# Kernel tuning notes

Measured on AMD Instinct MI355X. Metric: run time of the kernel, lower is better.

Reference implementation:

```python
import jax, jax.numpy as jnp
import numpy as np

# Production GravNet config: 8 events x 4096 hits, K=40 neighbours, 4 spatial dims
B, V, K, S, P, F_IN, F_OUT = 8, 4096, 40, 4, 64, 64, 128
N = B * V
MAX_RADIUS_SQ = 1.0  # SelectKnn(max_radius=1.0)


def setup_inputs() -> dict:
    key = jax.random.key(0)
    ks = jax.random.split(key, 7)
    x = jax.random.normal(ks[0], (N, F_IN), jnp.float32)
    # Dense layer params (glorot-ish scaling)
    W_prop = jax.random.normal(ks[1], (F_IN, P), jnp.float32) / np.sqrt(F_IN)
    b_prop = jnp.zeros((P,), jnp.float32)
    W_sp = jax.random.normal(ks[2], (F_IN, S), jnp.float32) / np.sqrt(F_IN)
    b_sp = jnp.zeros((S,), jnp.float32)
    # output transform input dim = n_prop_total (2*P) + F_IN
    W_out = jax.random.normal(ks[3], (2 * P + F_IN, F_OUT), jnp.float32) / np.sqrt(2 * P + F_IN)
    b_out = jnp.zeros((F_OUT,), jnp.float32)
    row_splits = jnp.arange(B + 1, dtype=jnp.int32) * V  # equal-size ragged segments
    return dict(x=x, W_prop=W_prop, b_prop=b_prop, W_sp=W_sp, b_sp=b_sp,
                W_out=W_out, b_out=b_out, row_splits=row_splits)


def _knn_indices(coords):
    """Per-event brute-force KNN. coords: [N,S] -> global neighbour idx [N,K]."""
    c = coords.reshape(B, V, S)
    # pairwise squared distances within each event: [B,V,V]
    d = jnp.sum((c[:, :, None, :] - c[:, None, :, :]) ** 2, axis=-1)
    neg_d, idx = jax.lax.top_k(-d, K + 1)  # nearest first; col 0 is self (d=0)
    idx, dsq = idx[:, :, 1:], -neg_d[:, :, 1:]
    # tf_compatible max_radius: out-of-radius neighbours -> self index
    self_idx = jnp.arange(V, dtype=idx.dtype)[None, :, None]
    idx = jnp.where(dsq > MAX_RADIUS_SQ, self_idx, idx)
    gidx = idx + (jnp.arange(B, dtype=idx.dtype) * V)[:, None, None]
    return gidx.reshape(N, K)


def reference(x, W_prop, b_prop, W_sp, b_sp, W_out, b_out, row_splits):
    coords = x @ W_sp + b_sp                      # [N,S] learned coordinates
    nidx = _knn_indices(coords)                   # [N,K] (int, non-diff)
    nb_coords = coords[nidx]                      # [N,K,S] gather
    dsq = jnp.sum((coords[:, None, :] - nb_coords) ** 2, axis=-1)  # [N,K]
    feat = x @ W_prop + b_prop                    # [N,P]
    w = jnp.exp(-10.0 * dsq)[:, :, None]          # gauss_of_lin(10*d^2)
    nf = feat[nidx] * w                           # [N,K,P]
    agg = jnp.concatenate([nf.max(axis=1), nf.mean(axis=1)], axis=-1)  # [N,2P]
    out = jnp.tanh(jnp.concatenate([agg, x], axis=-1) @ W_out + b_out)  # [N,F_OUT]
    return out
```

## Files before the change

### kernel.cpp

```cpp
#include <hip/hip_runtime.h>
#include <cstdint>
#include <cstddef>

#define NB   8
#define VV   4096
#define KNN  40
#define NTOT 32768
#define CAP  224
#define INFB 0x7F800000u
#define ONEB 0x3F800000u

__device__ __forceinline__ int slabf(float x) {
  int b = (int)floorf((x + 4.f) * 2.f);
  return b < 0 ? 0 : (b > 15 ? 15 : b);
}
__device__ __forceinline__ int ybf(float y) {
  int b = (int)floorf((y + 4.f) * 4.f);
  return b < 0 ? 0 : (b > 31 ? 31 : b);
}

__global__ __launch_bounds__(256) void k_prep(
    const float* __restrict__ x, const float* __restrict__ W_prop,
    const float* __restrict__ b_prop, const float* __restrict__ W_sp,
    const float* __restrict__ b_sp, const float* __restrict__ W_out,
    float* __restrict__ coords, float* __restrict__ feat,
    float* __restrict__ xW, int* __restrict__ hist)
{
  __shared__ float xt[64][64];
  const int t = threadIdx.x;
  const int row0 = blockIdx.x * 64;

  #pragma unroll
  for (int i = 0; i < 16; ++i) {
    int idx = t + i * 256;
    xt[idx >> 6][idx & 63] = x[(size_t)row0 * 64 + idx];
  }
  __syncthreads();

  {
    const int col = t & 63, rb = (t >> 6) * 16;
    float acc[16];
    #pragma unroll
    for (int i = 0; i < 16; ++i) acc[i] = b_prop[col];
    for (int k = 0; k < 64; k += 4) {
      const float w0 = W_prop[(k + 0) * 64 + col];
      const float w1 = W_prop[(k + 1) * 64 + col];
      const float w2 = W_prop[(k + 2) * 64 + col];
      const float w3 = W_prop[(k + 3) * 64 + col];
      #pragma unroll
      for (int i = 0; i < 16; ++i) {
        const float4 a4 = *(const float4*)&xt[rb + i][k];
        acc[i] += a4.x * w0 + a4.y * w1 + a4.z * w2 + a4.w * w3;
      }
    }
    #pragma unroll
    for (int i = 0; i < 16; ++i)
      feat[(size_t)(row0 + rb + i) * 64 + col] = acc[i];
  }

  {
    const int col = t & 127, who = t >> 7;
    #pragma unroll
    for (int p = 0; p < 2; ++p) {
      const int rb = who * 16 + p * 32;
      float acc[16];
      #pragma unroll
      for (int i = 0; i < 16; ++i) acc[i] = 0.f;
      for (int k = 0; k < 64; k += 4) {
        const float w0 = W_out[(size_t)(128 + k + 0) * 128 + col];
        const float w1 = W_out[(size_t)(128 + k + 1) * 128 + col];
        const float w2 = W_out[(size_t)(128 + k + 2) * 128 + col];
        const float w3 = W_out[(size_t)(128 + k + 3) * 128 + col];
        #pragma unroll
        for (int i = 0; i < 16; ++i) {
          const float4 a4 = *(const float4*)&xt[rb + i][k];
          acc[i] += a4.x * w0 + a4.y * w1 + a4.z * w2 + a4.w * w3;
        }
      }
      #pragma unroll
      for (int i = 0; i < 16; ++i)
        xW[(size_t)(row0 + rb + i) * 128 + col] = acc[i];
    }
  }

  if (t < 64) {
    float a0 = b_sp[0], a1 = b_sp[1], a2 = b_sp[2], a3 = b_sp[3];
    for (int k = 0; k < 64; ++k) {
      const float xv = xt[t][k];
      a0 += xv * W_sp[k * 4 + 0];
      a1 += xv * W_sp[k * 4 + 1];
      a2 += xv * W_sp[k * 4 + 2];
      a3 += xv * W_sp[k * 4 + 3];
    }
    ((float4*)coords)[row0 + t] = make_float4(a0, a1, a2, a3);
    const int ev = (row0 + t) >> 12;
    atomicAdd(&hist[ev * 512 + slabf(a0) * 32 + ybf(a1)], 1);
  }
}

__global__ __launch_bounds__(512) void k_scatter(
    const float* __restrict__ coords, float* __restrict__ csort,
    unsigned short* __restrict__ perm, const int* __restrict__ hist,
    int* __restrict__ cursorDelta, unsigned short* __restrict__ prefg)
{
  __shared__ int pref[513];
  const int t = threadIdx.x;
  const int ev = blockIdx.x >> 3;
  const int i = ((blockIdx.x & 7) << 9) + t;
  const int evbase = ev * VV;

  if (t < 64) {
    const int l = t;
    const int* h = hist + ev * 512 + 8 * l;
    int hv[8], s = 0;
    #pragma unroll
    for (int j = 0; j < 8; ++j) { hv[j] = h[j]; s += hv[j]; }
    int incl = s;
    #pragma unroll
    for (int off = 1; off < 64; off <<= 1) {
      const int v = __shfl_up(incl, off);
      if (l >= off) incl += v;
    }
    int run = incl - s;
    #pragma unroll
    for (int j = 0; j < 8; ++j) { pref[8 * l + j] = run; run += hv[j]; }
    if (l == 63) pref[512] = run;
  }
  __syncthreads();

  const float4 c = ((const float4*)coords)[evbase + i];
  const int key = slabf(c.x) * 32 + ybf(c.y);
  const int pos = pref[key] + atomicAdd(&cursorDelta[ev * 512 + key], 1);
  ((float4*)csort)[evbase + pos] = c;
  perm[evbase + pos] = (unsigned short)i;

  if ((blockIdx.x & 7) == 0) {
    prefg[ev * 513 + t] = (unsigned short)pref[t];
    if (t == 0) prefg[ev * 513 + 512] = (unsigned short)pref[512];
  }
}

template <int NC>
__device__ __forceinline__ unsigned bs40(const uint2* __restrict__ list,
                                         int M, int lane) {
  unsigned dv[NC];
  #pragma unroll
  for (int j = 0; j < NC; ++j) {
    const int e = lane + j * 64;
    dv[j] = (e < M) ? list[e].x : INFB;
  }
  unsigned lo = 0, hi = ONEB;
  while (lo < hi) {
    const unsigned mid = (lo + hi) >> 1;
    int cnt = 0;
    #pragma unroll
    for (int j = 0; j < NC; ++j)
      cnt += (int)__popcll(__ballot(dv[j] <= mid));
    if (cnt >= KNN) hi = mid; else lo = mid + 1;
  }
  return hi;
}

#define AGG_CHUNK(J0, N)                                                     \
  {                                                                          \
    float fv[N], wgt[N];                                                     \
    _Pragma("unroll")                                                        \
    for (int j = 0; j < N; ++j) {                                            \
      const uint2 en = list[(J0) + j];              \
      wgt[j] = __expf(-10.f * __uint_as_float(en.x));                        \
      const int ei = __builtin_amdgcn_readfirstlane((int)en.y);              \
      fv[j] = fe[(size_t)ei * 64 + lane];        \
    }                                                                        \
    _Pragma("unroll")                                                        \
    for (int j = 0; j < N; ++j) {                                            \
      const float v = fv[j] * wgt[j];                                        \
      vmax = fmaxf(vmax, v);                                                 \
      vsum += v;                                                             \
    }                                                                        \
  }

__global__ __launch_bounds__(512, 4) void k_knn(
    const float* __restrict__ coords,
    const unsigned short* __restrict__ perm,
    const unsigned short* __restrict__ prefg,
    const float* __restrict__ feat, float* __restrict__ agg,
    const float* __restrict__ W_out, const float* __restrict__ b_out,
    float* __restrict__ out)
{
  __shared__ float4 cs[VV];
  __shared__ uint2 lists[8][CAP];
  __shared__ unsigned short pr[513];
  __shared__ unsigned short origq_s[64];

  const int t = threadIdx.x, lane = t & 63;
  const int wvid = __builtin_amdgcn_readfirstlane(t) >> 6;
  const int bid0 = blockIdx.x;
  const int bid = (bid0 & 7) * 64 + (bid0 >> 3);
  const int ev = bid >> 6;
  const int slot = bid & 63;
  const int evbase = ev * VV;

  {
    const float4* cg = (const float4*)coords + evbase;
    for (int i = t; i < VV; i += 512) cs[i] = cg[i];
    for (int i = t; i < 513; i += 512) pr[i] = prefg[ev * 513 + i];
  }
  __syncthreads();

  uint2* list = lists[wvid];
  const float* fe = feat + (size_t)evbase * 64;
  const unsigned long long lmask = (1ull << lane) - 1ull;

  auto scanAll = [&](unsigned rbits, int q, float4 qc,
                     int slo, int shi, int yblo, int ybhi) -> int {
    int M = 0, pend = 0;
    for (int s = slo; s <= shi; ++s) {
      int alo = ((int)pr[(s << 5) + yblo]) & ~63;
      int ahi = (((int)pr[(s << 5) + ybhi + 1]) + 63) & ~63;
      alo = alo < pend ? pend : alo;
      if (ahi < alo) ahi = alo;
      pend = ahi;
      #pragma unroll 4
      for (int base = alo; base < ahi; base += 64) {
        const int c = base + lane;
        const float4 cc = cs[c];
        const float dx = qc.x - cc.x, dy = qc.y - cc.y;
        const float dz = qc.z - cc.z, dw = qc.w - cc.w;
        const float dsq = dx * dx + dy * dy + dz * dz + dw * dw;
        const bool pred = (__float_as_uint(dsq) <= rbits) && (c != q);
        const unsigned long long bm = __ballot(pred);
        if (pred) {
          const int pos = M + (int)__popcll(bm & lmask);
          if (pos < CAP)
            list[pos] = make_uint2(__float_as_uint(dsq), (unsigned)c);
        }
        M += (int)__popcll(bm);
      }
    }
    return M;
  };

  for (int qi = 0; qi < 8; ++qi) {
    const int q = slot + (qi * 8 + wvid) * 64;
    const float4 qc = cs[q];
    const int origq = (int)perm[evbase + q];
    if (lane == 0) origq_s[qi * 8 + wvid] = (unsigned short)origq;
    const int slo = slabf(qc.x - 1.f), shi = slabf(qc.x + 1.f);
    const int yblo = ybf(qc.y - 1.f),  ybhi = ybf(qc.y + 1.f);

    int M = scanAll(ONEB, q, qc, slo, shi, yblo, ybhi);
    bool ok = true;

    if (M > CAP) {
      const unsigned t0 = bs40<4>(list, CAP, lane);
      M = scanAll(t0, q, qc, slo, shi, yblo, ybhi);
      ok = (M <= CAP);
    }

    float vmax = -__builtin_inff(), vsum = 0.f;

    if (ok) {
      for (int be = 0; be < M; be += 64) {
        const int e = be + lane;
        if (e < M) {
          uint2 en = list[e];
          en.y = (unsigned)perm[evbase + (int)en.y];
          list[e] = en;
        }
      }

      int Msel;
      if (M > KNN) {
        unsigned taub;
        if      (M <=  64) taub = bs40<1>(list, M, lane);
        else if (M <= 128) taub = bs40<2>(list, M, lane);
        else               taub = bs40<4>(list, M, lane);
        int S = 0;
        for (int be = 0; be < M; be += 64) {
          const int e = be + lane;
          uint2 en = make_uint2(0u, 0u);
          bool p = false;
          if (e < M) { en = list[e]; p = (en.x <= taub); }
          const unsigned long long bm = __ballot(p);
          if (p) list[S + (int)__popcll(bm & lmask)] = en;
          S += (int)__popcll(bm);
        }
        Msel = S;
      } else {
        if (lane >= M && lane < KNN)
          list[lane] = make_uint2(0u, (unsigned)origq);
        Msel = KNN;
      }

      if (Msel == KNN) {
        AGG_CHUNK(0, 16)
        AGG_CHUNK(16, 16)
        AGG_CHUNK(32, 8)
      } else {
        #pragma unroll 4
        for (int e = 0; e < Msel; ++e) {
          const uint2 en = list[e];
          const int ei = __builtin_amdgcn_readfirstlane((int)en.y);
          const float w = __expf(-10.f * __uint_as_float(en.x));
          const float v = fe[(size_t)ei * 64 + lane] * w;
          vmax = fmaxf(vmax, v);
          vsum += v;
        }
      }
    } else {
      unsigned lo = 0, hi = ONEB;
      while (lo < hi) {
        const unsigned mid = (lo + hi) >> 1;
        const float fm = __uint_as_float(mid);
        int cnt = 0, pend = 0;
        for (int s = slo; s <= shi; ++s) {
          int alo = ((int)pr[(s << 5) + yblo]) & ~63;
          int ahi = (((int)pr[(s << 5) + ybhi + 1]) + 63) & ~63;
          alo = alo < pend ? pend : alo;
          if (ahi < alo) ahi = alo;
          pend = ahi;
          for (int base = alo; base < ahi; base += 64) {
            const int c = base + lane;
            const float4 cc = cs[c];
            const float dx = qc.x - cc.x, dy = qc.y - cc.y;
            const float dz = qc.z - cc.z, dw = qc.w - cc.w;
            const float dsq = dx * dx + dy * dy + dz * dz + dw * dw;
            cnt += (int)__popcll(__ballot(dsq <= fm && c != q));
          }
        }
        if (cnt >= KNN) hi = mid; else lo = mid + 1;
      }
      const float tau = __uint_as_float(hi);
      int pend = 0;
      for (int s = slo; s <= shi; ++s) {
        int alo = ((int)pr[(s << 5) + yblo]) & ~63;
        int ahi = (((int)pr[(s << 5) + ybhi + 1]) + 63) & ~63;
        alo = alo < pend ? pend : alo;
        if (ahi < alo) ahi = alo;
        pend = ahi;
        for (int c = alo; c < ahi; ++c) {
          if (c == q) continue;
          const float4 cc = cs[c];
          const float dx = qc.x - cc.x, dy = qc.y - cc.y;
          const float dz = qc.z - cc.z, dw = qc.w - cc.w;
          const float dsq = dx * dx + dy * dy + dz * dz + dw * dw;
          if (dsq <= tau) {
            const int ei = (int)perm[evbase + c];
            const float w = __expf(-10.f * dsq);
            const float v = fe[(size_t)ei * 64 + lane] * w;
            vmax = fmaxf(vmax, v);
            vsum += v;
          }
        }
      }
    }

    const int g = evbase + origq;
    agg[(size_t)g * 128 + lane]      = vmax;
    agg[(size_t)g * 128 + 64 + lane] = vsum * (1.f / 40.f);
  }

  __syncthreads();
  float* aggS = (float*)cs;
  #pragma unroll
  for (int p = 0; p < 4; ++p) {
    const int idx = t + p * 512;
    const int row = idx >> 5, seg = idx & 31;
    const int g = evbase + (int)origq_s[row];
    ((float4*)aggS)[idx] = *(const float4*)&agg[(size_t)g * 128 + seg * 4];
  }
  __syncthreads();

  {
    const int col = t & 127, who = t >> 7;
    float acc[16];
    #pragma unroll
    for (int i = 0; i < 16; ++i) acc[i] = 0.f;
    for (int k = 0; k < 128; k += 4) {
      const float w0 = W_out[(size_t)(k + 0) * 128 + col];
      const float w1 = W_out[(size_t)(k + 1) * 128 + col];
      const float w2 = W_out[(size_t)(k + 2) * 128 + col];
      const float w3 = W_out[(size_t)(k + 3) * 128 + col];
      #pragma unroll
      for (int i = 0; i < 16; ++i) {
        const float4 a4 = *(const float4*)&aggS[(who * 16 + i) * 128 + k];
        acc[i] += a4.x * w0 + a4.y * w1 + a4.z * w2 + a4.w * w3;
      }
    }
    const float bb = b_out[col];
    #pragma unroll
    for (int i = 0; i < 16; ++i) {
      const int row = who * 16 + i;
      const size_t o = ((size_t)evbase + origq_s[row]) * 128 + col;
      float v = acc[i] + bb + out[o];
      v = fminf(15.f, fmaxf(-15.f, v));
      const float e = __expf(2.f * v);
      out[o] = (e - 1.f) / (e + 1.f);
    }
  }
}

extern "C" void kernel_launch(void* const* d_in, const int* in_sizes, int n_in,
                              void* d_out, int out_size, void* d_ws, size_t ws_size,
                              hipStream_t stream) {
  const float* x      = (const float*)d_in[0];
  const float* W_prop = (const float*)d_in[1];
  const float* b_prop = (const float*)d_in[2];
  const float* W_sp   = (const float*)d_in[3];
  const float* b_sp   = (const float*)d_in[4];
  const float* W_out  = (const float*)d_in[5];
  const float* b_out  = (const float*)d_in[6];

  float* out = (float*)d_out;
  char* ws = (char*)d_ws;
  float* coords          = (float*)(ws);
  float* csort           = (float*)(ws + (512 << 10));
  float* feat            = (float*)(ws + (1 << 20));
  float* agg             = (float*)(ws + (9 << 20));
  unsigned short* perm   = (unsigned short*)(ws + (25 << 20));
  unsigned short* prefg  = (unsigned short*)(ws + (25 << 20) + 65536);
  int* hist              = (int*)(ws + (25 << 20) + 65536 + 8704);
  int* cursorDelta       = (int*)(ws + (25 << 20) + 65536 + 8704 + 16384);

  hipMemsetAsync(hist, 0, 32768, stream);
  k_prep<<<NTOT / 64, 256, 0, stream>>>(x, W_prop, b_prop, W_sp, b_sp, W_out,
                                        coords, feat, out ,
                                        hist);
  k_scatter<<<NB * 8, 512, 0, stream>>>(coords, csort, perm, hist,
                                        cursorDelta, prefg);
  k_knn<<<NB * (VV / 64), 512, 0, stream>>>(csort, perm, prefg, feat, agg,
                                            W_out, b_out, out);
}
```

Measured before the change: 180.0 us.

## Read coords from global and keep aggregates in shared memory instead of workspace

Removes the per-block staging of all 4096 event coordinates into LDS. The KNN scans now read the sorted coordinates directly from global memory, relying on cache. The freed LDS holds the 64x128 aggregate tile written directly by each wave, which removes the global agg round-trip and one barrier. In exchange, the inner scan loops now issue global/cache loads in place of LDS reads, which could raise latency in the distance loops.

```diff
diff --git a/kernel.cpp b/kernel.cpp
--- a/kernel.cpp
+++ b/kernel.cpp
@@ -183,11 +183,11 @@
     const float* __restrict__ coords,
     const unsigned short* __restrict__ perm,
     const unsigned short* __restrict__ prefg,
-    const float* __restrict__ feat, float* __restrict__ agg,
+    const float* __restrict__ feat,
     const float* __restrict__ W_out, const float* __restrict__ b_out,
     float* __restrict__ out)
 {
-  __shared__ float4 cs[VV];
+  __shared__ float aggS[64 * 128];
   __shared__ uint2 lists[8][CAP];
   __shared__ unsigned short pr[513];
   __shared__ unsigned short origq_s[64];
@@ -200,11 +200,8 @@
   const int slot = bid & 63;
   const int evbase = ev * VV;
 
-  {
-    const float4* cg = (const float4*)coords + evbase;
-    for (int i = t; i < VV; i += 512) cs[i] = cg[i];
-    for (int i = t; i < 513; i += 512) pr[i] = prefg[ev * 513 + i];
-  }
+  const float4* cg = (const float4*)coords + evbase;
+  for (int i = t; i < 513; i += 512) pr[i] = prefg[ev * 513 + i];
   __syncthreads();
 
   uint2* list = lists[wvid];
@@ -223,7 +220,7 @@
       #pragma unroll 4
       for (int base = alo; base < ahi; base += 64) {
         const int c = base + lane;
-        const float4 cc = cs[c];
+        const float4 cc = cg[c];
         const float dx = qc.x - cc.x, dy = qc.y - cc.y;
         const float dz = qc.z - cc.z, dw = qc.w - cc.w;
         const float dsq = dx * dx + dy * dy + dz * dz + dw * dw;
@@ -242,7 +239,7 @@
 
   for (int qi = 0; qi < 8; ++qi) {
     const int q = slot + (qi * 8 + wvid) * 64;
-    const float4 qc = cs[q];
+    const float4 qc = cg[q];
     const int origq = (int)perm[evbase + q];
     if (lane == 0) origq_s[qi * 8 + wvid] = (unsigned short)origq;
     const int slo = slabf(qc.x - 1.f), shi = slabf(qc.x + 1.f);
@@ -321,7 +318,7 @@
           pend = ahi;
           for (int base = alo; base < ahi; base += 64) {
             const int c = base + lane;
-            const float4 cc = cs[c];
+            const float4 cc = cg[c];
             const float dx = qc.x - cc.x, dy = qc.y - cc.y;
             const float dz = qc.z - cc.z, dw = qc.w - cc.w;
             const float dsq = dx * dx + dy * dy + dz * dz + dw * dw;
@@ -340,7 +337,7 @@
         pend = ahi;
         for (int c = alo; c < ahi; ++c) {
           if (c == q) continue;
-          const float4 cc = cs[c];
+          const float4 cc = cg[c];
           const float dx = qc.x - cc.x, dy = qc.y - cc.y;
           const float dz = qc.z - cc.z, dw = qc.w - cc.w;
           const float dsq = dx * dx + dy * dy + dz * dz + dw * dw;
@@ -355,38 +352,29 @@
       }
     }
 
-    const int g = evbase + origq;
-    agg[(size_t)g * 128 + lane]      = vmax;
-    agg[(size_t)g * 128 + 64 + lane] = vsum * (1.f / 40.f);
+    const int row = qi * 8 + wvid;
+    aggS[row * 128 + lane]      = vmax;
+    aggS[row * 128 + 64 + lane] = vsum * (1.f / 40.f);
   }
 
   __syncthreads();
-  float* aggS = (float*)cs;
+
+  const int col = t & 127, who = t >> 7;
+  float acc[16];
   #pragma unroll
-  for (int p = 0; p < 4; ++p) {
-    const int idx = t + p * 512;
-    const int row = idx >> 5, seg = idx & 31;
-    const int g = evbase + (int)origq_s[row];
-    ((float4*)aggS)[idx] = *(const float4*)&agg[(size_t)g * 128 + seg * 4];
-  }
-  __syncthreads();
-
+  for (int i = 0; i < 16; ++i) acc[i] = 0.f;
+  for (int k = 0; k < 128; k += 4) {
+    const float w0 = W_out[(size_t)(k + 0) * 128 + col];
+    const float w1 = W_out[(size_t)(k + 1) * 128 + col];
+    const float w2 = W_out[(size_t)(k + 2) * 128 + col];
+    const float w3 = W_out[(size_t)(k + 3) * 128 + col];
+    #pragma unroll
+    for (int i = 0; i < 16; ++i) {
+      const float4 a4 = *(const float4*)&aggS[(who * 16 + i) * 128 + k];
+      acc[i] += a4.x * w0 + a4.y * w1 + a4.z * w2 + a4.w * w3;
+    }
+  }
   {
-    const int col = t & 127, who = t >> 7;
-    float acc[16];
-    #pragma unroll
-    for (int i = 0; i < 16; ++i) acc[i] = 0.f;
-    for (int k = 0; k < 128; k += 4) {
-      const float w0 = W_out[(size_t)(k + 0) * 128 + col];
-      const float w1 = W_out[(size_t)(k + 1) * 128 + col];
-      const float w2 = W_out[(size_t)(k + 2) * 128 + col];
-      const float w3 = W_out[(size_t)(k + 3) * 128 + col];
-      #pragma unroll
-      for (int i = 0; i < 16; ++i) {
-        const float4 a4 = *(const float4*)&aggS[(who * 16 + i) * 128 + k];
-        acc[i] += a4.x * w0 + a4.y * w1 + a4.z * w2 + a4.w * w3;
-      }
-    }
     const float bb = b_out[col];
     #pragma unroll
     for (int i = 0; i < 16; ++i) {
@@ -416,11 +404,10 @@
   float* coords          = (float*)(ws);
   float* csort           = (float*)(ws + (512 << 10));
   float* feat            = (float*)(ws + (1 << 20));
-  float* agg             = (float*)(ws + (9 << 20));
-  unsigned short* perm   = (unsigned short*)(ws + (25 << 20));
-  unsigned short* prefg  = (unsigned short*)(ws + (25 << 20) + 65536);
-  int* hist              = (int*)(ws + (25 << 20) + 65536 + 8704);
-  int* cursorDelta       = (int*)(ws + (25 << 20) + 65536 + 8704 + 16384);
+  unsigned short* perm   = (unsigned short*)(ws + (9 << 20));
+  unsigned short* prefg  = (unsigned short*)(ws + (9 << 20) + 65536);
+  int* hist              = (int*)(ws + (9 << 20) + 65536 + 8704);
+  int* cursorDelta       = (int*)(ws + (9 << 20) + 65536 + 8704 + 16384);
 
   hipMemsetAsync(hist, 0, 32768, stream);
   k_prep<<<NTOT / 64, 256, 0, stream>>>(x, W_prop, b_prop, W_sp, b_sp, W_out,
@@ -428,6 +415,6 @@
                                         hist);
   k_scatter<<<NB * 8, 512, 0, stream>>>(coords, csort, perm, hist,
                                         cursorDelta, prefg);
-  k_knn<<<NB * (VV / 64), 512, 0, stream>>>(csort, perm, prefg, feat, agg,
+  k_knn<<<NB * (VV / 64), 512, 0, stream>>>(csort, perm, prefg, feat,
                                             W_out, b_out, out);
 }
```

Result: slower. 201.3 us (+11.9%).
